# Kernel tuning notes

Measured on AMD Instinct MI355X. Metric: run time of the kernel, lower is better.

The kernel has to match this reference:

```python
import jax, jax.numpy as jnp
import numpy as np

LS = (0, 1, 2, 3)          # l values of irreps_in1 and irreps_in2
LMAX_OUT = 3               # max l of target irreps
E = 20000                  # number of edges
C = 16                     # channels (uvu multiplicity)


def _build_sparse_cg(seed=0):
    """Build flattened sparse CG structure: mu_1, mu_2, mu_3 (sorted by mu_3
    within each path), cg values, per-path weight indices. The sparsity
    pattern follows the real-SH selection rule |m1+m2| == |m3|; values are
    synthetic stand-ins for wigner_3j * path_weight (same op structure)."""
    rng = np.random.default_rng(seed)
    offs = np.concatenate([[0], np.cumsum([2 * l + 1 for l in LS])])
    mu1l, mu2l, mu3l, cgl, wil = [], [], [], [], []
    off3 = 0
    path = 0
    for i, l1 in enumerate(LS):
        for j, l2 in enumerate(LS):
            for l3 in range(abs(l1 - l2), min(l1 + l2, LMAX_OUT) + 1):
                d1, d2, d3 = 2 * l1 + 1, 2 * l2 + 1, 2 * l3 + 1
                m1 = np.arange(d1) - l1
                m2 = np.arange(d2) - l2
                m3 = np.arange(d3) - l3
                M1, M2, M3 = np.meshgrid(m1, m2, m3, indexing='ij')
                i1, i2, i3 = np.nonzero(np.abs(M1 + M2) == np.abs(M3))
                vals = (rng.standard_normal(i1.size) / np.sqrt(d3)).astype(np.float32)
                order = np.argsort(i3, kind='stable')  # sort nnz by mu3
                mu1l.append(i1[order] + offs[i])
                mu2l.append(i2[order] + offs[j])
                mu3l.append(i3[order] + off3)
                cgl.append(vals[order])
                wil.append(np.full(i1.size, path, np.int32))
                off3 += d3
                path += 1
    return (np.concatenate(mu1l).astype(np.int32),
            np.concatenate(mu2l).astype(np.int32),
            np.concatenate(mu3l).astype(np.int32),
            np.concatenate(cgl),
            np.concatenate(wil),
            off3, path)


def setup_inputs() -> dict:
    key = jax.random.key(0)
    k1, k2, k3 = jax.random.split(key, 3)
    mu1, mu2, mu3, cg, widx, dim3, n_paths = _build_sparse_cg()
    dim_in = sum(2 * l + 1 for l in LS)  # 16
    x = jax.random.normal(k1, (E, dim_in, C), dtype=jnp.float32)
    y = jax.random.normal(k2, (E, dim_in), dtype=jnp.float32)
    weights = jax.random.normal(k3, (C, n_paths), dtype=jnp.float32)
    return {
        'x': x, 'y': y,
        'cg_coeffs': jnp.asarray(cg), 'weights': weights,
        'mu_1': jnp.asarray(mu1), 'mu_2': jnp.asarray(mu2), 'mu_3': jnp.asarray(mu3),
        'weight_indices': jnp.asarray(widx),
        'dim3': dim3,
    }


def reference(x, y, cg_coeffs, weights, mu_1, mu_2, mu_3, weight_indices, dim3):
    # Gather per-nonzero operands: out[e,mu3,c] += cg * x[e,mu1,c] * y[e,mu2] * w[c,path]
    xg = x[:, mu_1, :]                                # [E, K, C]
    yg = y[:, mu_2]                                   # [E, K]
    wk = weights[:, weight_indices].T                 # [K, C]
    vals = xg * yg[:, :, None] * (cg_coeffs[:, None] * wk)[None]  # [E, K, C]
    # scatter-add over mu_3 (segment ids on leading axis)
    out = jax.ops.segment_sum(jnp.swapaxes(vals, 0, 1), mu_3, num_segments=dim3)
    return jnp.swapaxes(out, 0, 1)                    # [E, dim3, C]
```

## Files before the change

kernel.cpp:

```cpp
#include <hip/hip_runtime.h>

#define TPB 256
#define NP  34
#define D3  156
#define NNZ 832
#define DIN 16
#define NC  16

struct CGStruct {
    unsigned char mu1[NNZ];
    unsigned char mu2[NNZ];
    unsigned char rowlen[D3];
    unsigned char rowpath[D3];
};

constexpr CGStruct build_cg() {
    CGStruct s{};
    int offs[4] = {0, 1, 4, 9};
    int off3 = 0, path = 0, k = 0;
    for (int i = 0; i < 4; ++i) {
        int l1 = i;
        for (int j = 0; j < 4; ++j) {
            int l2 = j;
            int lo = l1 - l2; if (lo < 0) lo = -lo;
            int hi = l1 + l2; if (hi > 3) hi = 3;
            for (int l3 = lo; l3 <= hi; ++l3) {
                int d1 = 2 * l1 + 1, d2 = 2 * l2 + 1, d3 = 2 * l3 + 1;
                for (int i3 = 0; i3 < d3; ++i3) {
                    int cnt = 0;
                    for (int i1 = 0; i1 < d1; ++i1)
                        for (int i2 = 0; i2 < d2; ++i2) {
                            int m12 = (i1 - l1) + (i2 - l2);
                            if (m12 < 0) m12 = -m12;
                            int m3 = i3 - l3; if (m3 < 0) m3 = -m3;
                            if (m12 == m3) {
                                s.mu1[k] = (unsigned char)(i1 + offs[i]);
                                s.mu2[k] = (unsigned char)(i2 + offs[j]);
                                ++k; ++cnt;
                            }
                        }
                    s.rowlen[off3 + i3]  = (unsigned char)cnt;
                    s.rowpath[off3 + i3] = (unsigned char)path;
                }
                off3 += d3;
                ++path;
            }
        }
    }
    return s;
}

constexpr CGStruct CGS = build_cg();

__global__ __launch_bounds__(TPB)
void tp_kernel(const float* __restrict__ x, const float* __restrict__ y,
               const float* __restrict__ cg, const float* __restrict__ wts,
               float* __restrict__ out, int E)
{
    __shared__ float wsh[NP * NC];
    for (int i = threadIdx.x; i < NP * NC; i += TPB) {
        int p = i >> 4, c = i & 15;
        wsh[i] = wts[c * NP + p];
    }
    __syncthreads();

    const int t = threadIdx.x;
    const int c = t & 15;
    const int e = blockIdx.x * (TPB / NC) + (t >> 4);
    if (e >= E) return;

    float xv[DIN], yv[DIN];
    const float* xp = x + (size_t)e * (DIN * NC) + c;
    const float* yp = y + (size_t)e * DIN;
#pragma unroll
    for (int d = 0; d < DIN; ++d) xv[d] = xp[d * NC];
#pragma unroll
    for (int d = 0; d < DIN; ++d) yv[d] = yp[d];

    float* outp = out + (size_t)e * (D3 * NC) + c;

    int k = 0;
#pragma unroll
    for (int r = 0; r < D3; ++r) {
        float acc = 0.f;
#pragma unroll
        for (int q = 0; q < CGS.rowlen[r]; ++q) {
            acc += cg[k] * yv[CGS.mu2[k]] * xv[CGS.mu1[k]];
            ++k;
        }
        outp[(size_t)r * NC] = acc * wsh[CGS.rowpath[r] * NC + c];
    }
}

extern "C" void kernel_launch(void* const* d_in, const int* in_sizes, int n_in,
                              void* d_out, int out_size, void* d_ws, size_t ws_size,
                              hipStream_t stream)
{
    const float* x   = (const float*)d_in[0];
    const float* y   = (const float*)d_in[1];
    const float* cg  = (const float*)d_in[2];
    const float* wts = (const float*)d_in[3];
    float* out = (float*)d_out;

    const int E = in_sizes[1] / DIN;

    dim3 grid((E * NC + TPB - 1) / TPB), block(TPB);
    hipLaunchKernelGGL(tp_kernel, grid, block, 0, stream,
                       x, y, cg, wts, out, E);
}
```

Baseline: 232.0 us.

## Split output rows across four thread groups per edge

Each edge is now handled by four 16-thread groups instead of one. Each group computes an interleaved quarter of the 156 output rows, picked through a switch on compile-time templated row sets. This gives four times as many threads, cutting the serial per-thread instruction stream and raising parallelism. In exchange every group reloads the same x and y values, and the switch on rq costs extra code size. Since rq equals t>>6 and a 64-wide wavefront covers exactly one rq value, there is no divergence within a wavefront.

```diff
diff --git a/kernel.cpp b/kernel.cpp
--- a/kernel.cpp
+++ b/kernel.cpp
@@ -6,12 +6,15 @@
 #define NNZ 832
 #define DIN 16
 #define NC  16
+#define RSPLIT 4
+#define EPB (TPB / (NC * RSPLIT))
 
 struct CGStruct {
-    unsigned char mu1[NNZ];
-    unsigned char mu2[NNZ];
-    unsigned char rowlen[D3];
-    unsigned char rowpath[D3];
+    unsigned char  mu1[NNZ];
+    unsigned char  mu2[NNZ];
+    unsigned char  rowlen[D3];
+    unsigned char  rowpath[D3];
+    unsigned short rowk[D3];
 };
 
 constexpr CGStruct build_cg() {
@@ -27,6 +30,7 @@
             for (int l3 = lo; l3 <= hi; ++l3) {
                 int d1 = 2 * l1 + 1, d2 = 2 * l2 + 1, d3 = 2 * l3 + 1;
                 for (int i3 = 0; i3 < d3; ++i3) {
+                    s.rowk[off3 + i3] = (unsigned short)k;
                     int cnt = 0;
                     for (int i1 = 0; i1 < d1; ++i1)
                         for (int i2 = 0; i2 < d2; ++i2) {
@@ -52,6 +56,26 @@
 
 constexpr CGStruct CGS = build_cg();
 
+template<int Q>
+__device__ __forceinline__ void do_rows(const float* __restrict__ cg,
+                                        const float* __restrict__ wrow,
+                                        float* __restrict__ outp,
+                                        const float (&xv)[DIN],
+                                        const float (&yv)[DIN])
+{
+#pragma unroll
+    for (int r = Q; r < D3; r += RSPLIT) {
+        float acc = 0.f;
+        int k = CGS.rowk[r];
+#pragma unroll
+        for (int q = 0; q < CGS.rowlen[r]; ++q) {
+            acc += cg[k] * yv[CGS.mu2[k]] * xv[CGS.mu1[k]];
+            ++k;
+        }
+        outp[(size_t)r * NC] = acc * wrow[CGS.rowpath[r] * NC];
+    }
+}
+
 __global__ __launch_bounds__(TPB)
 void tp_kernel(const float* __restrict__ x, const float* __restrict__ y,
                const float* __restrict__ cg, const float* __restrict__ wts,
@@ -59,14 +83,16 @@
 {
     __shared__ float wsh[NP * NC];
     for (int i = threadIdx.x; i < NP * NC; i += TPB) {
-        int p = i >> 4, c = i & 15;
-        wsh[i] = wts[c * NP + p];
+        int p = i >> 4, cc = i & 15;
+        wsh[i] = wts[cc * NP + p];
     }
     __syncthreads();
 
-    const int t = threadIdx.x;
-    const int c = t & 15;
-    const int e = blockIdx.x * (TPB / NC) + (t >> 4);
+    const int t  = threadIdx.x;
+    const int c  = t & 15;
+    const int el = (t >> 4) & (EPB - 1);
+    const int rq = t >> 6;
+    const int e  = blockIdx.x * EPB + el;
     if (e >= E) return;
 
     float xv[DIN], yv[DIN];
@@ -78,17 +104,13 @@
     for (int d = 0; d < DIN; ++d) yv[d] = yp[d];
 
     float* outp = out + (size_t)e * (D3 * NC) + c;
+    const float* wrow = &wsh[c];
 
-    int k = 0;
-#pragma unroll
-    for (int r = 0; r < D3; ++r) {
-        float acc = 0.f;
-#pragma unroll
-        for (int q = 0; q < CGS.rowlen[r]; ++q) {
-            acc += cg[k] * yv[CGS.mu2[k]] * xv[CGS.mu1[k]];
-            ++k;
-        }
-        outp[(size_t)r * NC] = acc * wsh[CGS.rowpath[r] * NC + c];
+    switch (rq) {
+        case 0: do_rows<0>(cg, wrow, outp, xv, yv); break;
+        case 1: do_rows<1>(cg, wrow, outp, xv, yv); break;
+        case 2: do_rows<2>(cg, wrow, outp, xv, yv); break;
+        case 3: do_rows<3>(cg, wrow, outp, xv, yv); break;
     }
 }
 
@@ -104,7 +126,7 @@
 
     const int E = in_sizes[1] / DIN;
 
-    dim3 grid((E * NC + TPB - 1) / TPB), block(TPB);
+    dim3 grid((E + EPB - 1) / EPB), block(TPB);
     hipLaunchKernelGGL(tp_kernel, grid, block, 0, stream,
                        x, y, cg, wts, out, E);
 }
```

Result: no change. 232.3 us (+0.1%).
